# Kernel optimization log

Measured on AMD Instinct MI355X. Metric: run time of the kernel, lower is better.

## Reference

```python
import jax, jax.numpy as jnp
import numpy as np

L = 4096   # seq len (Lq == Lk, self-attention)
B = 8      # batch
D = 1024   # d_model
H = 16     # num heads
BUCKET = 32
FUTURE = 0


def setup_inputs() -> dict:
    key = jax.random.key(0)
    ks = jax.random.split(key, 9)
    q = jax.random.normal(ks[0], (L, B, D), jnp.float32)
    k = jax.random.normal(ks[1], (L, B, D), jnp.float32)
    v = jax.random.normal(ks[2], (L, B, D), jnp.float32)
    # one random element per bucket of size BUCKET (deterministic stand-in for
    # the module's no_grad sample_index); pin first sample to 0 so no query row
    # is fully masked under the causal mask.
    nb = L // BUCKET
    offs = jax.random.randint(ks[3], (nb,), 0, BUCKET)
    sampled_index = (jnp.arange(nb, dtype=jnp.int64) * BUCKET + offs).at[0].set(0)
    key_length = jax.random.randint(ks[4], (B,), L // 2, L + 1).astype(jnp.int64)
    # nn.MultiheadAttention params
    in_proj_weight = jax.random.normal(ks[5], (3 * D, D), jnp.float32) * 0.02
    in_proj_bias = jax.random.normal(ks[6], (3 * D,), jnp.float32) * 0.02
    out_w = jax.random.normal(ks[7], (D, D), jnp.float32) * 0.02
    out_b = jax.random.normal(ks[8], (D,), jnp.float32) * 0.02
    return {"q": q, "k": k, "v": v, "key_length": key_length,
            "sampled_index": sampled_index, "in_proj_weight": in_proj_weight,
            "in_proj_bias": in_proj_bias, "out_w": out_w, "out_b": out_b}


def reference(q, k, v, key_length, sampled_index, in_proj_weight, in_proj_bias, out_w, out_b):
    S = sampled_index.shape[0]
    dh = D // H
    # bucket-sampled gather of keys/values: [S, B, D]
    ks_ = k[sampled_index]
    vs_ = v[sampled_index]
    # modify_key_length: number of sampled indices inside each sequence's valid span
    mkl = jnp.sum((sampled_index[None, :] < key_length[:, None]).astype(jnp.int32), axis=1)  # [B]
    key_padding = jnp.arange(S)[None, :] >= mkl[:, None]                                      # [B, S] True = pad
    # causal mask on sampled indices: query i may attend to sample s iff i + future >= s
    causal = (jnp.arange(L)[:, None] + FUTURE) < sampled_index[None, :]                       # [Lq, S] True = masked
    mask = causal[None, None, :, :] | key_padding[:, None, None, :]                           # [B, 1, Lq, S]
    # in-projection (torch linear: x @ W.T + b)
    Wq, Wk, Wv = jnp.split(in_proj_weight, 3, axis=0)
    bq, bk, bv = jnp.split(in_proj_bias, 3)
    qp = (q @ Wq.T + bq).reshape(L, B, H, dh)
    kp = (ks_ @ Wk.T + bk).reshape(S, B, H, dh)
    vp = (vs_ @ Wv.T + bv).reshape(S, B, H, dh)
    scale = 1.0 / np.sqrt(dh).astype(np.float32)
    scores = jnp.einsum('qbhd,kbhd->bhqk', qp, kp) * scale
    scores = jnp.where(mask, -jnp.inf, scores)
    attn = jax.nn.softmax(scores, axis=-1)
    ctx = jnp.einsum('bhqk,kbhd->qbhd', attn, vp).reshape(L, B, D)
    return ctx @ out_w.T + out_b
```

## Files before the change

kernel.cpp:

```cpp
#include <hip/hip_runtime.h>
#include <hip/hip_bf16.h>

#define L_SEQ 4096
#define BATCH 8
#define DMODEL 1024
#define NHEAD 16
#define DHEAD 64
#define NSAMP 128

typedef __attribute__((ext_vector_type(8))) short short8;
typedef __attribute__((ext_vector_type(4))) float f32x4;

static __device__ __forceinline__ unsigned short f2bf(float f) {
    union { float f; unsigned int u; } x; x.f = f;
    unsigned int r = (x.u + 0x7fffu + ((x.u >> 16) & 1u)) >> 16;
    return (unsigned short)r;
}

static __device__ __forceinline__ void gld_lds16(const unsigned short* g,
                                                 unsigned short* l) {
    __builtin_amdgcn_global_load_lds(
        (const __attribute__((address_space(1))) void*)g,
        (__attribute__((address_space(3))) void*)l, 16, 0, 0);
}

__global__ void conv_bf16_kernel(const float* __restrict__ src,
                                 unsigned short* __restrict__ dst, int n4) {
    int idx = blockIdx.x * blockDim.x + threadIdx.x;
    if (idx < n4) {
        float4 v = ((const float4*)src)[idx];
        uint2 pk;
        pk.x = (unsigned)f2bf(v.x) | ((unsigned)f2bf(v.y) << 16);
        pk.y = (unsigned)f2bf(v.z) | ((unsigned)f2bf(v.w) << 16);
        ((uint2*)dst)[idx] = pk;
    }
}

__global__ void gather_bf16_kernel(const float* __restrict__ src,
                                   const int* __restrict__ smp,
                                   unsigned short* __restrict__ dst, int total8) {
    int idx = blockIdx.x * blockDim.x + threadIdx.x;
    if (idx < total8) {
        int s = idx >> 10;
        int rem = idx & 1023;
        const float* g = src + (size_t)smp[s] * (BATCH * DMODEL) + rem * 8;
        float4 v0 = *(const float4*)g;
        float4 v1 = *(const float4*)(g + 4);
        uint4 pk;
        pk.x = (unsigned)f2bf(v0.x) | ((unsigned)f2bf(v0.y) << 16);
        pk.y = (unsigned)f2bf(v0.z) | ((unsigned)f2bf(v0.w) << 16);
        pk.z = (unsigned)f2bf(v1.x) | ((unsigned)f2bf(v1.y) << 16);
        pk.w = (unsigned)f2bf(v1.z) | ((unsigned)f2bf(v1.w) << 16);
        *(uint4*)&dst[(size_t)idx * 8] = pk;
    }
}

__global__ void mkl_kernel(const int* __restrict__ smp,
                           const int* __restrict__ klen, int* __restrict__ mkl) {
    int b = threadIdx.x;
    if (b < BATCH) {
        int kl = klen[b];
        int c = 0;
        for (int s = 0; s < NSAMP; ++s) c += (smp[s] < kl) ? 1 : 0;
        mkl[b] = c;
    }
}

template <bool OUT_F32>
static __device__ __forceinline__ void gemm_body(
    const unsigned short* __restrict__ A, const unsigned short* __restrict__ Bw,
    const float* __restrict__ bias, void* __restrict__ Cp,
    int m0, int n0, int N, int K,
    unsigned short* lA, unsigned short* lB) {
    const int t = threadIdx.x;
    const int wave = t >> 6;
    const int lane = t & 63;
    const int l16 = lane & 15;
    const int quad = lane >> 4;
    const int wm = (wave >> 1) * 64;
    const int wn = (wave & 1) * 64;

    f32x4 acc[4][4];
    #pragma unroll
    for (int i = 0; i < 4; ++i)
        #pragma unroll
        for (int j = 0; j < 4; ++j)
            acc[i][j] = f32x4{0.f, 0.f, 0.f, 0.f};

    const int lin0 = t * 8;
    const int wbase = (t & ~63) * 8;

    for (int k0 = 0; k0 < K; k0 += 64) {
        #pragma unroll
        for (int p = 0; p < 4; ++p) {
            int lin = p * 2048 + lin0;
            int row = lin >> 6, col = lin & 63;
            gld_lds16(A + (size_t)(m0 + row) * K + k0 + col, lA + p * 2048 + wbase);
        }
        #pragma unroll
        for (int p = 0; p < 4; ++p) {
            int lin = p * 2048 + lin0;
            int row = lin >> 6, col = lin & 63;
            gld_lds16(Bw + (size_t)(n0 + row) * K + k0 + col, lB + p * 2048 + wbase);
        }
        __syncthreads();

        #pragma unroll
        for (int kk = 0; kk < 64; kk += 32) {
            short8 af[4], bfr[4];
            #pragma unroll
            for (int mt = 0; mt < 4; ++mt)
                af[mt] = *(const short8*)&lA[(wm + mt * 16 + l16) * 64 + kk + quad * 8];
            #pragma unroll
            for (int nt = 0; nt < 4; ++nt)
                bfr[nt] = *(const short8*)&lB[(wn + nt * 16 + l16) * 64 + kk + quad * 8];
            #pragma unroll
            for (int mt = 0; mt < 4; ++mt)
                #pragma unroll
                for (int nt = 0; nt < 4; ++nt)
                    acc[mt][nt] = __builtin_amdgcn_mfma_f32_16x16x32_bf16(
                        af[mt], bfr[nt], acc[mt][nt], 0, 0, 0);
        }
        __syncthreads();
    }

    #pragma unroll
    for (int mt = 0; mt < 4; ++mt) {
        #pragma unroll
        for (int nt = 0; nt < 4; ++nt) {
            int col = n0 + wn + nt * 16 + l16;
            float bv = bias[col];
            #pragma unroll
            for (int r = 0; r < 4; ++r) {
                int row = m0 + wm + mt * 16 + quad * 4 + r;
                float val = acc[mt][nt][r] + bv;
                if (OUT_F32)
                    ((float*)Cp)[(size_t)row * N + col] = val;
                else
                    ((unsigned short*)Cp)[(size_t)row * N + col] = f2bf(val);
            }
        }
    }
}

__global__ __launch_bounds__(256) void gemm_bf16out(
    const unsigned short* __restrict__ A, const unsigned short* __restrict__ Bw,
    const float* __restrict__ bias, unsigned short* __restrict__ C, int N, int K) {
    __shared__ __align__(16) unsigned short lA[128 * 64];
    __shared__ __align__(16) unsigned short lB[128 * 64];
    gemm_body<false>(A, Bw, bias, C, blockIdx.x * 128, blockIdx.y * 128, N, K, lA, lB);
}

__global__ __launch_bounds__(256) void gemm_f32out(
    const unsigned short* __restrict__ A, const unsigned short* __restrict__ Bw,
    const float* __restrict__ bias, float* __restrict__ C, int N, int K) {
    __shared__ __align__(16) unsigned short lA[128 * 64];
    __shared__ __align__(16) unsigned short lB[128 * 64];
    gemm_body<true>(A, Bw, bias, C, blockIdx.x * 128, blockIdx.y * 128, N, K, lA, lB);
}

__global__ __launch_bounds__(256) void gemm_kv(
    const unsigned short* __restrict__ Ak, const unsigned short* __restrict__ Av,
    const unsigned short* __restrict__ Bk, const unsigned short* __restrict__ Bv,
    const float* __restrict__ bk, const float* __restrict__ bv,
    unsigned short* __restrict__ Ck, unsigned short* __restrict__ Cv) {
    __shared__ __align__(16) unsigned short lA[128 * 64];
    __shared__ __align__(16) unsigned short lB[128 * 64];
    if (blockIdx.z == 0)
        gemm_body<false>(Ak, Bk, bk, Ck, blockIdx.x * 128, blockIdx.y * 128,
                         DMODEL, DMODEL, lA, lB);
    else
        gemm_body<false>(Av, Bv, bv, Cv, blockIdx.x * 128, blockIdx.y * 128,
                         DMODEL, DMODEL, lA, lB);
}

#define KST 72
#define VST 136
__global__ __launch_bounds__(256) void attn_kernel(
    const unsigned short* __restrict__ qp,
    const unsigned short* __restrict__ kp,
    const unsigned short* __restrict__ vp,
    const int* __restrict__ smp_g,
    const int* __restrict__ mkl_g,
    unsigned short* __restrict__ ctx)
{
    __shared__ __align__(16) unsigned short kbuf[NSAMP * KST];
    __shared__ __align__(16) unsigned short vT[64 * VST];
    __shared__ __align__(16) unsigned short pbuf[4][16 * VST];
    __shared__ int smp_s[NSAMP];

    const int t = threadIdx.x;
    const int b = blockIdx.y >> 4, h = blockIdx.y & 15;
    const int wave = t >> 6, lane = t & 63;
    const int l16 = lane & 15, quad = lane >> 4;
    const int Lbase = blockIdx.x * 256;
    const int mkl_b = mkl_g[b];

    #pragma unroll
    for (int p = 0; p < 4; ++p) {
        int c = p * 256 + t;
        int s = c >> 3, d0 = (c & 7) * 8;
        *(uint4*)&kbuf[s * KST + d0] =
            *(const uint4*)&kp[((size_t)(s * BATCH + b)) * DMODEL + h * 64 + d0];
    }
    #pragma unroll
    for (int p = 0; p < 4; ++p) {
        int c = p * 256 + t;
        int s = c >> 3, d0 = (c & 7) * 8;
        uint4 pk = *(const uint4*)&vp[((size_t)(s * BATCH + b)) * DMODEL + h * 64 + d0];
        const unsigned short* e = (const unsigned short*)&pk;
        #pragma unroll
        for (int j = 0; j < 8; ++j) vT[(d0 + j) * VST + s] = e[j];
    }
    if (t < NSAMP) smp_s[t] = smp_g[t];
    __syncthreads();

    short8 kf[8][2];
    #pragma unroll
    for (int nt = 0; nt < 8; ++nt) {
        kf[nt][0] = *(const short8*)&kbuf[(nt * 16 + l16) * KST + quad * 8];
        kf[nt][1] = *(const short8*)&kbuf[(nt * 16 + l16) * KST + 32 + quad * 8];
    }

    const float scale = 0.125f;

    for (int qt = 0; qt < 4; ++qt) {
        const int l0 = Lbase + wave * 64 + qt * 16;

        short8 aq0, aq1;
        {
            const unsigned short* qrow =
                qp + ((size_t)(l0 + l16) * BATCH + b) * DMODEL + h * 64;
            aq0 = *(const short8*)&qrow[quad * 8];
            aq1 = *(const short8*)&qrow[32 + quad * 8];
        }

        f32x4 sc[8];
        #pragma unroll
        for (int nt = 0; nt < 8; ++nt) sc[nt] = f32x4{0.f, 0.f, 0.f, 0.f};
        #pragma unroll
        for (int nt = 0; nt < 8; ++nt) {
            sc[nt] = __builtin_amdgcn_mfma_f32_16x16x32_bf16(aq0, kf[nt][0], sc[nt], 0, 0, 0);
            sc[nt] = __builtin_amdgcn_mfma_f32_16x16x32_bf16(aq1, kf[nt][1], sc[nt], 0, 0, 0);
        }

        #pragma unroll
        for (int nt = 0; nt < 8; ++nt) {
            int s = nt * 16 + l16;
            bool pad = (s >= mkl_b);
            int si = smp_s[s];
            #pragma unroll
            for (int r = 0; r < 4; ++r) {
                int lrow = l0 + quad * 4 + r;
                float v = sc[nt][r] * scale;
                if (pad || si > lrow) v = -INFINITY;
                sc[nt][r] = v;
            }
        }
        #pragma unroll
        for (int r = 0; r < 4; ++r) {
            float mx = sc[0][r];
            #pragma unroll
            for (int nt = 1; nt < 8; ++nt) mx = fmaxf(mx, sc[nt][r]);
            #pragma unroll
            for (int off = 1; off < 16; off <<= 1) mx = fmaxf(mx, __shfl_xor(mx, off));
            float sm = 0.f;
            #pragma unroll
            for (int nt = 0; nt < 8; ++nt) {
                float e = __expf(sc[nt][r] - mx);
                sc[nt][r] = e;
                sm += e;
            }
            #pragma unroll
            for (int off = 1; off < 16; off <<= 1) sm += __shfl_xor(sm, off);
            float inv = 1.0f / sm;
            #pragma unroll
            for (int nt = 0; nt < 8; ++nt) sc[nt][r] *= inv;
        }

        #pragma unroll
        for (int nt = 0; nt < 8; ++nt)
            #pragma unroll
            for (int r = 0; r < 4; ++r)
                pbuf[wave][(quad * 4 + r) * VST + nt * 16 + l16] = f2bf(sc[nt][r]);

        f32x4 oc[4];
        #pragma unroll
        for (int dt = 0; dt < 4; ++dt) oc[dt] = f32x4{0.f, 0.f, 0.f, 0.f};
        #pragma unroll
        for (int s0 = 0; s0 < 128; s0 += 32) {
            short8 ap = *(const short8*)&pbuf[wave][l16 * VST + s0 + quad * 8];
            #pragma unroll
            for (int dt = 0; dt < 4; ++dt) {
                short8 bv = *(const short8*)&vT[(dt * 16 + l16) * VST + s0 + quad * 8];
                oc[dt] = __builtin_amdgcn_mfma_f32_16x16x32_bf16(ap, bv, oc[dt], 0, 0, 0);
            }
        }

        #pragma unroll
        for (int dt = 0; dt < 4; ++dt)
            #pragma unroll
            for (int r = 0; r < 4; ++r) {
                int lrow = l0 + quad * 4 + r;
                ctx[((size_t)lrow * BATCH + b) * DMODEL + h * 64 + dt * 16 + l16] =
                    f2bf(oc[dt][r]);
            }
    }
}

extern "C" void kernel_launch(void* const* d_in, const int* in_sizes, int n_in,
                              void* d_out, int out_size, void* d_ws, size_t ws_size,
                              hipStream_t stream) {
    const float* q    = (const float*)d_in[0];
    const float* k    = (const float*)d_in[1];
    const float* v    = (const float*)d_in[2];
    const int*   klen = (const int*)d_in[3];
    const int*   smp  = (const int*)d_in[4];
    const float* ipw  = (const float*)d_in[5];
    const float* ipb  = (const float*)d_in[6];
    const float* ow   = (const float*)d_in[7];
    const float* ob   = (const float*)d_in[8];
    float* out = (float*)d_out;

    char* ws = (char*)d_ws;
    size_t off = 0;
    auto alloc = [&](size_t bytes) -> void* {
        void* p = ws + off;
        off += (bytes + 255) & ~(size_t)255;
        return p;
    };
    unsigned short* w_bf  = (unsigned short*)alloc((size_t)3 * 1024 * 1024 * 2);
    unsigned short* ow_bf = (unsigned short*)alloc((size_t)1024 * 1024 * 2);
    unsigned short* ks_bf = (unsigned short*)alloc((size_t)NSAMP * BATCH * DMODEL * 2);
    unsigned short* vs_bf = (unsigned short*)alloc((size_t)NSAMP * BATCH * DMODEL * 2);
    unsigned short* q_bf  = (unsigned short*)alloc((size_t)L_SEQ * BATCH * DMODEL * 2);
    unsigned short* qp    = (unsigned short*)alloc((size_t)L_SEQ * BATCH * DMODEL * 2);
    unsigned short* kpp   = (unsigned short*)alloc((size_t)NSAMP * BATCH * DMODEL * 2);
    unsigned short* vpp   = (unsigned short*)alloc((size_t)NSAMP * BATCH * DMODEL * 2);
    int*            mkl   = (int*)alloc(256);
    unsigned short* ctx = q_bf;

    conv_bf16_kernel<<<32768, 256, 0, stream>>>(q, q_bf, L_SEQ * BATCH * DMODEL / 4);
    conv_bf16_kernel<<<3072, 256, 0, stream>>>(ipw, w_bf, 3 * 1024 * 1024 / 4);
    conv_bf16_kernel<<<1024, 256, 0, stream>>>(ow, ow_bf, 1024 * 1024 / 4);
    gather_bf16_kernel<<<512, 256, 0, stream>>>(k, smp, ks_bf, NSAMP * BATCH * DMODEL / 8);
    gather_bf16_kernel<<<512, 256, 0, stream>>>(v, smp, vs_bf, NSAMP * BATCH * DMODEL / 8);
    mkl_kernel<<<1, 64, 0, stream>>>(smp, klen, mkl);

    gemm_bf16out<<<dim3(256, 8), 256, 0, stream>>>(q_bf, w_bf, ipb, qp, DMODEL, DMODEL);
    gemm_kv<<<dim3(8, 8, 2), 256, 0, stream>>>(
        ks_bf, vs_bf, w_bf + (size_t)1024 * 1024, w_bf + (size_t)2 * 1024 * 1024,
        ipb + 1024, ipb + 2048, kpp, vpp);

    attn_kernel<<<dim3(L_SEQ / 256, BATCH * NHEAD), 256, 0, stream>>>(
        qp, kpp, vpp, smp, mkl, ctx);

    gemm_f32out<<<dim3(256, 8), 256, 0, stream>>>(ctx, ow_bf, ob, out, DMODEL, DMODEL);
}
```

Baseline: 659.2 us.

## Replace Q and output projection GEMMs with 256x256-tile pipelined kernel

```diff
diff --git a/kernel.cpp b/kernel.cpp
--- a/kernel.cpp
+++ b/kernel.cpp
@@ -143,22 +143,6 @@
     }
 }
 
-__global__ __launch_bounds__(256) void gemm_bf16out(
-    const unsigned short* __restrict__ A, const unsigned short* __restrict__ Bw,
-    const float* __restrict__ bias, unsigned short* __restrict__ C, int N, int K) {
-    __shared__ __align__(16) unsigned short lA[128 * 64];
-    __shared__ __align__(16) unsigned short lB[128 * 64];
-    gemm_body<false>(A, Bw, bias, C, blockIdx.x * 128, blockIdx.y * 128, N, K, lA, lB);
-}
-
-__global__ __launch_bounds__(256) void gemm_f32out(
-    const unsigned short* __restrict__ A, const unsigned short* __restrict__ Bw,
-    const float* __restrict__ bias, float* __restrict__ C, int N, int K) {
-    __shared__ __align__(16) unsigned short lA[128 * 64];
-    __shared__ __align__(16) unsigned short lB[128 * 64];
-    gemm_body<true>(A, Bw, bias, C, blockIdx.x * 128, blockIdx.y * 128, N, K, lA, lB);
-}
-
 __global__ __launch_bounds__(256) void gemm_kv(
     const unsigned short* __restrict__ Ak, const unsigned short* __restrict__ Av,
     const unsigned short* __restrict__ Bk, const unsigned short* __restrict__ Bv,
@@ -172,6 +156,104 @@
     else
         gemm_body<false>(Av, Bv, bv, Cv, blockIdx.x * 128, blockIdx.y * 128,
                          DMODEL, DMODEL, lA, lB);
+}
+
+#define GNT 32
+
+template <bool OUT_F32>
+__global__ __launch_bounds__(512, 2) void gemm256_kernel(
+    const unsigned short* __restrict__ A, const unsigned short* __restrict__ Bw,
+    const float* __restrict__ bias, void* __restrict__ Cp)
+{
+    __shared__ __align__(16) unsigned short ls[4][2][8192];
+
+    const int bid = blockIdx.x;
+    const int swz = (bid & 7) * 64 + (bid >> 3);
+    const int m0 = (swz >> 2) * 256;
+    const int n0 = (swz & 3) * 256;
+
+    const int t = threadIdx.x;
+    const int wave = t >> 6, lane = t & 63;
+    const int l16 = lane & 15, quad = lane >> 4;
+    const int wm = wave >> 2, wn = wave & 3;
+    const int wb = wave * 512;
+
+    const int srow = t >> 2;
+    const int scol = (t & 3) * 8;
+    const unsigned short* a0 = A + (size_t)(m0 + srow) * DMODEL + scol;
+    const unsigned short* a1 = a0 + (size_t)128 * DMODEL;
+    const unsigned short* b0 = Bw + (size_t)(n0 + srow) * DMODEL + scol;
+    const unsigned short* b1 = b0 + (size_t)128 * DMODEL;
+
+    #define STAGE(tk, s) do {                                   \
+        gld_lds16(a0 + (tk) * 32, &ls[s][0][wb]);               \
+        gld_lds16(a1 + (tk) * 32, &ls[s][0][4096 + wb]);        \
+        gld_lds16(b0 + (tk) * 32, &ls[s][1][wb]);               \
+        gld_lds16(b1 + (tk) * 32, &ls[s][1][4096 + wb]);        \
+    } while (0)
+
+    STAGE(0, 0); STAGE(1, 1); STAGE(2, 2);
+
+    f32x4 acc[8][4];
+    #pragma unroll
+    for (int i = 0; i < 8; ++i)
+        #pragma unroll
+        for (int j = 0; j < 4; ++j)
+            acc[i][j] = f32x4{0.f, 0.f, 0.f, 0.f};
+
+    const int aoff = (wm * 128 + l16) * 32 + quad * 8;
+    const int boff = (wn * 64 + l16) * 32 + quad * 8;
+
+    #pragma unroll
+    for (int tk = 0; tk < GNT; ++tk) {
+        if (tk < GNT - 2)
+            asm volatile("s_waitcnt vmcnt(8)" ::: "memory");
+        else if (tk == GNT - 2)
+            asm volatile("s_waitcnt vmcnt(4)" ::: "memory");
+        else
+            asm volatile("s_waitcnt vmcnt(0)" ::: "memory");
+        __builtin_amdgcn_s_barrier();
+
+        if (tk + 3 < GNT) STAGE(tk + 3, (tk + 3) & 3);
+
+        const unsigned short* As = &ls[tk & 3][0][0];
+        const unsigned short* Bs = &ls[tk & 3][1][0];
+        short8 af[8], bq[4];
+        #pragma unroll
+        for (int nt = 0; nt < 4; ++nt)
+            bq[nt] = *(const short8*)&Bs[boff + nt * 512];
+        #pragma unroll
+        for (int mt = 0; mt < 8; ++mt)
+            af[mt] = *(const short8*)&As[aoff + mt * 512];
+
+        __builtin_amdgcn_s_setprio(1);
+        #pragma unroll
+        for (int mt = 0; mt < 8; ++mt)
+            #pragma unroll
+            for (int nt = 0; nt < 4; ++nt)
+                acc[mt][nt] = __builtin_amdgcn_mfma_f32_16x16x32_bf16(
+                    af[mt], bq[nt], acc[mt][nt], 0, 0, 0);
+        __builtin_amdgcn_s_setprio(0);
+    }
+    #undef STAGE
+
+    #pragma unroll
+    for (int mt = 0; mt < 8; ++mt) {
+        #pragma unroll
+        for (int nt = 0; nt < 4; ++nt) {
+            int col = n0 + wn * 64 + nt * 16 + l16;
+            float bv = bias[col];
+            #pragma unroll
+            for (int r = 0; r < 4; ++r) {
+                int row = m0 + wm * 128 + mt * 16 + quad * 4 + r;
+                float val = acc[mt][nt][r] + bv;
+                if (OUT_F32)
+                    ((float*)Cp)[(size_t)row * DMODEL + col] = val;
+                else
+                    ((unsigned short*)Cp)[(size_t)row * DMODEL + col] = f2bf(val);
+            }
+        }
+    }
 }
 
 #define KST 72
@@ -347,7 +429,7 @@
     gather_bf16_kernel<<<512, 256, 0, stream>>>(v, smp, vs_bf, NSAMP * BATCH * DMODEL / 8);
     mkl_kernel<<<1, 64, 0, stream>>>(smp, klen, mkl);
 
-    gemm_bf16out<<<dim3(256, 8), 256, 0, stream>>>(q_bf, w_bf, ipb, qp, DMODEL, DMODEL);
+    gemm256_kernel<false><<<dim3(512), 512, 0, stream>>>(q_bf, w_bf, ipb, qp);
     gemm_kv<<<dim3(8, 8, 2), 256, 0, stream>>>(
         ks_bf, vs_bf, w_bf + (size_t)1024 * 1024, w_bf + (size_t)2 * 1024 * 1024,
         ipb + 1024, ipb + 2048, kpp, vpp);
@@ -355,5 +437,5 @@
     attn_kernel<<<dim3(L_SEQ / 256, BATCH * NHEAD), 256, 0, stream>>>(
         qp, kpp, vpp, smp, mkl, ctx);
 
-    gemm_f32out<<<dim3(256, 8), 256, 0, stream>>>(ctx, ow_bf, ob, out, DMODEL, DMODEL);
-}
+    gemm256_kernel<true><<<dim3(512), 512, 0, stream>>>(ctx, ow_bf, ob, out);
+}
```

After: 601.9 us. 1.1x faster.
